# Performance work log

Measured on AMD Instinct MI355X. Metric: run time of the kernel, lower is better.

## Reference

```python
import jax, jax.numpy as jnp
import numpy as np

B, S, E, N = 2, 2048, 768, 12
H = E // N

def setup_inputs() -> dict:
    key = jax.random.key(0)
    k1, k2, k3, k4, k5 = jax.random.split(key, 5)
    x = jax.random.normal(k1, (B, S, E), dtype=jnp.float32)
    Wqkv = jax.random.normal(k2, (E, 3 * E), dtype=jnp.float32) * (1.0 / np.sqrt(E))
    bqkv = jax.random.normal(k3, (3 * E,), dtype=jnp.float32) * 0.02
    Wproj = jax.random.normal(k4, (E, E), dtype=jnp.float32) * (1.0 / np.sqrt(E))
    bproj = jax.random.normal(k5, (E,), dtype=jnp.float32) * 0.02
    mask = jnp.tril(jnp.ones((S, S), dtype=jnp.int32))[None, None]  # (1,1,S,S) causal
    return {"mask": mask, "x": x, "Wqkv": Wqkv, "bqkv": bqkv, "Wproj": Wproj, "bproj": bproj}

def reference(mask, x, Wqkv, bqkv, Wproj, bproj):
    Bx, Sx, Ex = x.shape
    Hd = Ex // N
    qkv = x @ Wqkv + bqkv                       # (B,S,3E)
    q, k, v = jnp.split(qkv, 3, axis=-1)
    q = q.reshape(Bx, Sx, N, Hd).transpose(0, 2, 1, 3)  # (B,N,S,H)
    k = k.reshape(Bx, Sx, N, Hd).transpose(0, 2, 1, 3)
    v = v.reshape(Bx, Sx, N, Hd).transpose(0, 2, 1, 3)
    att = jnp.einsum('bnsh,bnth->bnst', q, k) / jnp.sqrt(jnp.float32(Hd))
    att = jnp.where(mask == 0, -jnp.inf, att)   # causal masked_fill
    p = jax.nn.softmax(att, axis=-1)            # dropout p=0.0 -> identity
    y = jnp.einsum('bnst,bnth->bnsh', p, v)     # (B,N,S,H)
    y = y.transpose(0, 2, 1, 3).reshape(Bx, Sx, Ex)
    return y @ Wproj + bproj
```

## Files before the change

### kernel.cpp

```cpp
#include <hip/hip_runtime.h>
#include <math.h>

#define S_LEN 2048
#define E_DIM 768
#define NHEAD 12
#define HDIM 64
#define BATCH 2
#define MROWS (BATCH * S_LEN)
#define KDIM E_DIM
#define NBN (BATCH * NHEAD)
#define NTASKS 768

typedef __attribute__((ext_vector_type(8))) short bf16x8;
typedef __attribute__((ext_vector_type(4))) float f32x4;

__device__ inline unsigned short f2bf(float f) {
    union { float f; unsigned u; } v; v.f = f;
    unsigned r = (v.u + 0x7FFFu + ((v.u >> 16) & 1u)) >> 16;
    return (unsigned short)r;
}

__global__ __launch_bounds__(256) void prep(
    const float* __restrict__ x, unsigned short* __restrict__ Xb,
    const float* __restrict__ Wqkv, unsigned short* __restrict__ WqkvT,
    const float* __restrict__ Wproj, unsigned short* __restrict__ WprojT)
{
    __shared__ float t[32][33];
    const int blk = blockIdx.x, tid = threadIdx.x;
    if (blk < 3072) {
        const int i = blk * 256 + tid;
        const float4 a = ((const float4*)x)[i];
        ushort4 o;
        o.x = f2bf(a.x); o.y = f2bf(a.y); o.z = f2bf(a.z); o.w = f2bf(a.w);
        ((ushort4*)Xb)[i] = o;
        return;
    }
    const float* W; unsigned short* WT; int N, bt;
    if (blk < 3072 + 1728) { bt = blk - 3072; N = 3 * E_DIM; W = Wqkv; WT = WqkvT; }
    else                   { bt = blk - 4800; N = E_DIM;     W = Wproj; WT = WprojT; }
    const int bx = bt % (N / 32), by = bt / (N / 32);
    const int k0 = by * 32, n0 = bx * 32;
    const int r = tid >> 3, c4 = (tid & 7) * 4;
    const float4 v = *(const float4*)&W[(size_t)(k0 + r) * N + n0 + c4];
    t[r][c4 + 0] = v.x; t[r][c4 + 1] = v.y; t[r][c4 + 2] = v.z; t[r][c4 + 3] = v.w;
    __syncthreads();
    ushort4 o;
    o.x = f2bf(t[c4 + 0][r]); o.y = f2bf(t[c4 + 1][r]);
    o.z = f2bf(t[c4 + 2][r]); o.w = f2bf(t[c4 + 3][r]);
    *(ushort4*)&WT[(size_t)(n0 + r) * KDIM + k0 + c4] = o;
}

template <int EPI, int BM, int BN>
__global__ __launch_bounds__(256, 3) void gemm_t(
    const unsigned short* __restrict__ A, const unsigned short* __restrict__ BT,
    const float* __restrict__ bias, void* __restrict__ out0,
    void* __restrict__ out1, void* __restrict__ out2, int Nn)
{
    constexpr int MF = BM / 32;
    constexpr int NF = BN / 32;
    __shared__ unsigned short As[BM * 64];
    __shared__ unsigned short Bs[BN * 64];
    const int tid = threadIdx.x;
    const int lane = tid & 63;
    const int wid = tid >> 6;
    const int lr = lane & 15, lg = lane >> 4;
    const int wr = wid >> 1, wc = wid & 1;
    const int m0 = blockIdx.y * BM;
    const int n0 = blockIdx.x * BN;
    const int srow = lane >> 3, scol = (lane & 7) * 8;

    f32x4 acc[MF][NF];
    #pragma unroll
    for (int i = 0; i < MF; ++i)
        #pragma unroll
        for (int j = 0; j < NF; ++j) acc[i][j] = (f32x4){0.f, 0.f, 0.f, 0.f};

    for (int k0 = 0; k0 < KDIM; k0 += 64) {
        __syncthreads();
        #pragma unroll
        for (int c = 0; c < MF; ++c) {
            const int chunk = wid * MF + c;
            const int row = chunk * 8 + srow;
            const unsigned short* ga = A + (size_t)(m0 + row) * KDIM + k0 + scol;
            __builtin_amdgcn_global_load_lds(
                (const __attribute__((address_space(1))) void*)ga,
                (__attribute__((address_space(3))) void*)&As[chunk * 512], 16, 0, 0);
        }
        #pragma unroll
        for (int c = 0; c < NF; ++c) {
            const int chunk = wid * NF + c;
            const int row = chunk * 8 + srow;
            const unsigned short* gb = BT + (size_t)(n0 + row) * KDIM + k0 + scol;
            __builtin_amdgcn_global_load_lds(
                (const __attribute__((address_space(1))) void*)gb,
                (__attribute__((address_space(3))) void*)&Bs[chunk * 512], 16, 0, 0);
        }
        __syncthreads();

        #pragma unroll
        for (int kk = 0; kk < 2; ++kk) {
            bf16x8 af[MF], bf[NF];
            #pragma unroll
            for (int mt = 0; mt < MF; ++mt)
                af[mt] = *(const bf16x8*)&As[(wr * (BM / 2) + mt * 16 + lr) * 64 + kk * 32 + lg * 8];
            #pragma unroll
            for (int nt = 0; nt < NF; ++nt)
                bf[nt] = *(const bf16x8*)&Bs[(wc * (BN / 2) + nt * 16 + lr) * 64 + kk * 32 + lg * 8];
            #pragma unroll
            for (int mt = 0; mt < MF; ++mt)
                #pragma unroll
                for (int nt = 0; nt < NF; ++nt)
                    acc[mt][nt] = __builtin_amdgcn_mfma_f32_16x16x32_bf16(
                        af[mt], bf[nt], acc[mt][nt], 0, 0, 0);
        }
    }

    #pragma unroll
    for (int mt = 0; mt < MF; ++mt) {
        const int rowbase = m0 + wr * (BM / 2) + mt * 16 + lg * 4;
        #pragma unroll
        for (int nt = 0; nt < NF; ++nt) {
            const int col = n0 + wc * (BN / 2) + nt * 16 + lr;
            if (EPI == 0) {
                float* O = (float*)out0;
                const float bv = bias[col];
                #pragma unroll
                for (int r = 0; r < 4; ++r)
                    O[(size_t)(rowbase + r) * Nn + col] = acc[mt][nt][r] + bv;
            } else {
                const int which = col / E_DIM;
                const int rem = col % E_DIM;
                const int head = rem >> 6, h = rem & 63;
                const float bv = bias[col];
                if (which == 2) {
                    const int b = rowbase >> 11, s0 = rowbase & (S_LEN - 1);
                    const int scolv = (s0 & ~63) | ((s0 & 63) ^ ((h & 7) << 3));
                    unsigned short* VT = (unsigned short*)out2;
                    ushort4 pk;
                    pk.x = f2bf(acc[mt][nt][0] + bv);
                    pk.y = f2bf(acc[mt][nt][1] + bv);
                    pk.z = f2bf(acc[mt][nt][2] + bv);
                    pk.w = f2bf(acc[mt][nt][3] + bv);
                    *(ushort4*)&VT[((size_t)(b * NHEAD + head) * HDIM + h) * S_LEN + scolv] = pk;
                } else {
                    unsigned short* dst = (which == 0) ? (unsigned short*)out0
                                                       : (unsigned short*)out1;
                    const float sc = (which == 0) ? 0.125f : 1.0f;
                    #pragma unroll
                    for (int r = 0; r < 4; ++r) {
                        const int m = rowbase + r;
                        const int b = m >> 11, s = m & (S_LEN - 1);
                        const int hh = (which == 1) ? (h ^ ((s & 7) << 3)) : h;
                        dst[(((size_t)(b * NHEAD + head) * S_LEN) + s) * HDIM + hh] =
                            f2bf((acc[mt][nt][r] + bv) * sc);
                    }
                }
            }
        }
    }
}

__global__ __launch_bounds__(256) void attn_mfma(
    const unsigned short* __restrict__ Qb, const unsigned short* __restrict__ Kb,
    const unsigned short* __restrict__ VTb, unsigned short* __restrict__ Y,
    float* __restrict__ ws_o, float* __restrict__ ws_l)
{
    __shared__ unsigned short Ks[2][64 * 64];
    __shared__ unsigned short Vt[2][64 * 64];
    __shared__ unsigned short Ps[4 * 16 * 64];
    __shared__ float Ls[4][16];

    const int tid = threadIdx.x;
    const int lane = tid & 63;
    const int wid = tid >> 6;
    const int lr = lane & 15;
    const int lg = lane >> 4;

    const int task = blockIdx.x;
    const int bn = task % NBN;
    const int rest = task / NBN;
    const int jj = rest & 15, half = rest >> 4;
    const int b = bn / NHEAD, n = bn % NHEAD;

    const unsigned short* Kg = Kb + (size_t)bn * S_LEN * HDIM;
    const unsigned short* Vg = VTb + (size_t)bn * HDIM * S_LEN;

    auto run_pass = [&](int qb, int t0, int t1, int mode) {
        const size_t qoff = ((size_t)bn * S_LEN + (qb * 64 + wid * 16 + lr)) * HDIM;
        const bf16x8 qB0 = *(const bf16x8*)(Qb + qoff + lg * 8);
        const bf16x8 qB1 = *(const bf16x8*)(Qb + qoff + 32 + lg * 8);

        f32x4 o[4];
        #pragma unroll
        for (int ht = 0; ht < 4; ++ht) o[ht] = (f32x4){0.f, 0.f, 0.f, 0.f};
        float lacc = 0.f;

        __syncthreads();
        #pragma unroll
        for (int e = 0; e < 2; ++e) {
            const int chunk = wid * 2 + e;
            __builtin_amdgcn_global_load_lds(
                (const __attribute__((address_space(1))) void*)
                    (Kg + (size_t)t0 * 4096 + chunk * 512 + lane * 8),
                (__attribute__((address_space(3))) void*)&Ks[0][chunk * 512], 16, 0, 0);
            __builtin_amdgcn_global_load_lds(
                (const __attribute__((address_space(1))) void*)
                    (Vg + (size_t)(chunk * 8 + (lane >> 3)) * S_LEN + t0 * 64 + (lane & 7) * 8),
                (__attribute__((address_space(3))) void*)&Vt[0][chunk * 512], 16, 0, 0);
        }

        int cur = 0;
        for (int t = t0; t < t1; ++t) {
            __syncthreads();
            if (t + 1 < t1) {
                #pragma unroll
                for (int e = 0; e < 2; ++e) {
                    const int chunk = wid * 2 + e;
                    __builtin_amdgcn_global_load_lds(
                        (const __attribute__((address_space(1))) void*)
                            (Kg + (size_t)(t + 1) * 4096 + chunk * 512 + lane * 8),
                        (__attribute__((address_space(3))) void*)&Ks[cur ^ 1][chunk * 512],
                        16, 0, 0);
                    __builtin_amdgcn_global_load_lds(
                        (const __attribute__((address_space(1))) void*)
                            (Vg + (size_t)(chunk * 8 + (lane >> 3)) * S_LEN + (t + 1) * 64
                                + (lane & 7) * 8),
                        (__attribute__((address_space(3))) void*)&Vt[cur ^ 1][chunk * 512],
                        16, 0, 0);
                }
            }

            const unsigned short* Kc = Ks[cur];
            f32x4 s[4];
            __builtin_amdgcn_s_setprio(1);
            #pragma unroll
            for (int ct = 0; ct < 4; ++ct) {
                const int kr = ct * 16 + lr;
                const int xo = (kr & 7) << 3;
                const bf16x8 kb0 = *(const bf16x8*)&Kc[kr * 64 + ((lg * 8) ^ xo)];
                const bf16x8 kb1 = *(const bf16x8*)&Kc[kr * 64 + ((32 + lg * 8) ^ xo)];
                f32x4 a = (f32x4){0.f, 0.f, 0.f, 0.f};
                a = __builtin_amdgcn_mfma_f32_16x16x32_bf16(kb0, qB0, a, 0, 0, 0);
                a = __builtin_amdgcn_mfma_f32_16x16x32_bf16(kb1, qB1, a, 0, 0, 0);
                s[ct] = a;
            }
            __builtin_amdgcn_s_setprio(0);

            if (t == qb) {
                const int q = qb * 64 + wid * 16 + lr;
                #pragma unroll
                for (int ct = 0; ct < 4; ++ct) {
                    #pragma unroll
                    for (int r = 0; r < 4; ++r) {
                        const int k = t * 64 + ct * 16 + lg * 4 + r;
                        if (k > q) s[ct][r] = -1e30f;
                    }
                }
            }

            unsigned short* Pw = Ps + wid * 1024;
            const int pxo = (lr & 7) << 3;
            #pragma unroll
            for (int ct = 0; ct < 4; ++ct) {
                const float p0 = __expf(s[ct][0] - 8.f);
                const float p1 = __expf(s[ct][1] - 8.f);
                const float p2 = __expf(s[ct][2] - 8.f);
                const float p3 = __expf(s[ct][3] - 8.f);
                lacc += (p0 + p1) + (p2 + p3);
                ushort4 pk;
                pk.x = f2bf(p0); pk.y = f2bf(p1); pk.z = f2bf(p2); pk.w = f2bf(p3);
                *(ushort4*)&Pw[lr * 64 + ((ct * 16 + lg * 4) ^ pxo)] = pk;
            }

            const unsigned short* Vc = Vt[cur];
            const bf16x8 pa0 = *(const bf16x8*)&Pw[lr * 64 + ((lg * 8) ^ pxo)];
            const bf16x8 pa1 = *(const bf16x8*)&Pw[lr * 64 + ((32 + lg * 8) ^ pxo)];
            __builtin_amdgcn_s_setprio(1);
            #pragma unroll
            for (int ht = 0; ht < 4; ++ht) {
                const int h = ht * 16 + lr;
                const int xo = (h & 7) << 3;
                const bf16x8 vb0 = *(const bf16x8*)&Vc[h * 64 + ((lg * 8) ^ xo)];
                const bf16x8 vb1 = *(const bf16x8*)&Vc[h * 64 + ((32 + lg * 8) ^ xo)];
                o[ht] = __builtin_amdgcn_mfma_f32_16x16x32_bf16(pa0, vb0, o[ht], 0, 0, 0);
                o[ht] = __builtin_amdgcn_mfma_f32_16x16x32_bf16(pa1, vb1, o[ht], 0, 0, 0);
            }
            __builtin_amdgcn_s_setprio(0);
            cur ^= 1;
        }

        lacc += __shfl_xor(lacc, 16, 64);
        lacc += __shfl_xor(lacc, 32, 64);

        if (mode == 2) {
            if (lg == 0) Ls[wid][lr] = lacc;
            const float4 lv = *(const float4*)&Ls[wid][lg * 4];
            const float invl[4] = {1.f / lv.x, 1.f / lv.y, 1.f / lv.z, 1.f / lv.w};
            #pragma unroll
            for (int r = 0; r < 4; ++r) {
                const int qrow = qb * 64 + wid * 16 + lg * 4 + r;
                unsigned short* yrow =
                    Y + ((size_t)(b * S_LEN + qrow)) * E_DIM + n * HDIM;
                #pragma unroll
                for (int ht = 0; ht < 4; ++ht)
                    yrow[ht * 16 + lr] = f2bf(o[ht][r] * invl[r]);
            }
        } else {
            const size_t m = (size_t)(bn * 16 + (qb - 16)) * 2 + mode;
            float* wo = ws_o + m * 4096;
            const int rowl = wid * 16 + lg * 4;
            #pragma unroll
            for (int ht = 0; ht < 4; ++ht)
                #pragma unroll
                for (int r = 0; r < 4; ++r)
                    wo[(rowl + r) * 64 + ht * 16 + lr] = o[ht][r];
            if (lg == 0) ws_l[m * 64 + wid * 16 + lr] = lacc;
        }
    };

    if (half == 0) {
        run_pass(31 - jj, 0, 16, 0);
    } else {
        run_pass(31 - jj, 16, 32 - jj, 1);
        run_pass(jj, 0, jj + 1, 2);
    }
}

__global__ __launch_bounds__(256) void attn_merge(
    const float* __restrict__ ws_o, const float* __restrict__ ws_l,
    unsigned short* __restrict__ Y)
{
    const int m = blockIdx.x;
    const int bn = m / 16, qb = 16 + (m % 16);
    const int b = bn / NHEAD, n = bn % NHEAD;
    const int tid = threadIdx.x;
    const int r = tid >> 2, h0 = (tid & 3) * 16;

    const float* o0 = ws_o + ((size_t)m * 2 + 0) * 4096 + r * 64 + h0;
    const float* o1 = ws_o + ((size_t)m * 2 + 1) * 4096 + r * 64 + h0;
    const float l = ws_l[((size_t)m * 2 + 0) * 64 + r] +
                    ws_l[((size_t)m * 2 + 1) * 64 + r];
    const float inv = 1.f / l;
    unsigned short* yrow =
        Y + ((size_t)(b * S_LEN + qb * 64 + r)) * E_DIM + n * HDIM + h0;
    #pragma unroll
    for (int q = 0; q < 16; q += 4) {
        const float4 a = *(const float4*)(o0 + q);
        const float4 c = *(const float4*)(o1 + q);
        ushort4 pk;
        pk.x = f2bf((a.x + c.x) * inv); pk.y = f2bf((a.y + c.y) * inv);
        pk.z = f2bf((a.z + c.z) * inv); pk.w = f2bf((a.w + c.w) * inv);
        *(ushort4*)&yrow[q] = pk;
    }
}

extern "C" void kernel_launch(void* const* d_in, const int* in_sizes, int n_in,
                              void* d_out, int out_size, void* d_ws, size_t ws_size,
                              hipStream_t stream) {
    const float* x     = (const float*)d_in[1];
    const float* Wqkv  = (const float*)d_in[2];
    const float* bqkv  = (const float*)d_in[3];
    const float* Wproj = (const float*)d_in[4];
    const float* bproj = (const float*)d_in[5];
    float* out = (float*)d_out;

    const size_t per = (size_t)BATCH * NHEAD * S_LEN * HDIM;
    unsigned short* Xb     = (unsigned short*)d_ws;
    unsigned short* WqkvT  = Xb + (size_t)MROWS * E_DIM;
    unsigned short* WprojT = WqkvT + (size_t)3 * E_DIM * E_DIM;
    unsigned short* Qb     = WprojT + (size_t)E_DIM * E_DIM;
    unsigned short* Kb     = Qb + per;
    unsigned short* VTb    = Kb + per;
    unsigned short* Yb     = VTb + per;
    float*          ws_o   = (float*)(Yb + (size_t)MROWS * E_DIM);
    float*          ws_l   = ws_o + (size_t)384 * 2 * 4096;

    prep<<<5376, 256, 0, stream>>>(x, Xb, Wqkv, WqkvT, Wproj, WprojT);
    gemm_t<1, 128, 96><<<dim3(3 * E_DIM / 96, MROWS / 128), 256, 0, stream>>>(
        Xb, WqkvT, bqkv, Qb, Kb, VTb, 3 * E_DIM);
    attn_mfma<<<NTASKS, 256, 0, stream>>>(Qb, Kb, VTb, Yb, ws_o, ws_l);
    attn_merge<<<384, 256, 0, stream>>>(ws_o, ws_l, Yb);
    gemm_t<0, 64, 64><<<dim3(E_DIM / 64, MROWS / 64), 256, 0, stream>>>(
        Yb, WprojT, bproj, out, nullptr, nullptr, E_DIM);
}
```

Measured before the change: 84.20 us.

## Split attention warps 2x2 over query and key halves with shared P tile

Reorganizes the attention block's four waves from one 16-row query strip each into a 2x2 grid: each wave handles 32 query rows against 32 of the 64 keys per tile. K and V fragments read from LDS are reused across two query groups, which cuts LDS read traffic per MFMA. Partial outputs from the two key-half waves are reduced through shared memory at the end, and row sums go through a small LDS buffer. This adds extra barriers and an LDS reduction per pass, plus a shared P tile written and read across waves.

```diff
diff --git a/kernel.cpp b/kernel.cpp
--- a/kernel.cpp
+++ b/kernel.cpp
@@ -165,16 +165,18 @@
     const unsigned short* __restrict__ VTb, unsigned short* __restrict__ Y,
     float* __restrict__ ws_o, float* __restrict__ ws_l)
 {
-    __shared__ unsigned short Ks[2][64 * 64];
-    __shared__ unsigned short Vt[2][64 * 64];
-    __shared__ unsigned short Ps[4 * 16 * 64];
-    __shared__ float Ls[4][16];
+    __shared__ unsigned short smem[5 * 4096];
+    __shared__ float Lbuf[2][2][32];
 
     const int tid = threadIdx.x;
     const int lane = tid & 63;
     const int wid = tid >> 6;
     const int lr = lane & 15;
     const int lg = lane >> 4;
+    const int wq = wid >> 1;
+    const int wk = wid & 1;
+
+    unsigned short* const Ps = smem + 16384;
 
     const int task = blockIdx.x;
     const int bn = task % NBN;
@@ -186,14 +188,21 @@
     const unsigned short* Vg = VTb + (size_t)bn * HDIM * S_LEN;
 
     auto run_pass = [&](int qb, int t0, int t1, int mode) {
-        const size_t qoff = ((size_t)bn * S_LEN + (qb * 64 + wid * 16 + lr)) * HDIM;
-        const bf16x8 qB0 = *(const bf16x8*)(Qb + qoff + lg * 8);
-        const bf16x8 qB1 = *(const bf16x8*)(Qb + qoff + 32 + lg * 8);
-
-        f32x4 o[4];
-        #pragma unroll
-        for (int ht = 0; ht < 4; ++ht) o[ht] = (f32x4){0.f, 0.f, 0.f, 0.f};
-        float lacc = 0.f;
+        bf16x8 qB[2][2];
+        #pragma unroll
+        for (int qg = 0; qg < 2; ++qg) {
+            const size_t qoff =
+                ((size_t)bn * S_LEN + (qb * 64 + wq * 32 + qg * 16 + lr)) * HDIM;
+            qB[qg][0] = *(const bf16x8*)(Qb + qoff + lg * 8);
+            qB[qg][1] = *(const bf16x8*)(Qb + qoff + 32 + lg * 8);
+        }
+
+        f32x4 o[4][2];
+        #pragma unroll
+        for (int ht = 0; ht < 4; ++ht)
+            #pragma unroll
+            for (int qg = 0; qg < 2; ++qg) o[ht][qg] = (f32x4){0.f, 0.f, 0.f, 0.f};
+        float lacc[2] = {0.f, 0.f};
 
         __syncthreads();
         #pragma unroll
@@ -202,11 +211,11 @@
             __builtin_amdgcn_global_load_lds(
                 (const __attribute__((address_space(1))) void*)
                     (Kg + (size_t)t0 * 4096 + chunk * 512 + lane * 8),
-                (__attribute__((address_space(3))) void*)&Ks[0][chunk * 512], 16, 0, 0);
+                (__attribute__((address_space(3))) void*)&smem[chunk * 512], 16, 0, 0);
             __builtin_amdgcn_global_load_lds(
                 (const __attribute__((address_space(1))) void*)
                     (Vg + (size_t)(chunk * 8 + (lane >> 3)) * S_LEN + t0 * 64 + (lane & 7) * 8),
-                (__attribute__((address_space(3))) void*)&Vt[0][chunk * 512], 16, 0, 0);
+                (__attribute__((address_space(3))) void*)&smem[8192 + chunk * 512], 16, 0, 0);
         }
 
         int cur = 0;
@@ -219,102 +228,156 @@
                     __builtin_amdgcn_global_load_lds(
                         (const __attribute__((address_space(1))) void*)
                             (Kg + (size_t)(t + 1) * 4096 + chunk * 512 + lane * 8),
-                        (__attribute__((address_space(3))) void*)&Ks[cur ^ 1][chunk * 512],
-                        16, 0, 0);
+                        (__attribute__((address_space(3))) void*)
+                            &smem[(cur ^ 1) * 4096 + chunk * 512], 16, 0, 0);
                     __builtin_amdgcn_global_load_lds(
                         (const __attribute__((address_space(1))) void*)
                             (Vg + (size_t)(chunk * 8 + (lane >> 3)) * S_LEN + (t + 1) * 64
                                 + (lane & 7) * 8),
-                        (__attribute__((address_space(3))) void*)&Vt[cur ^ 1][chunk * 512],
-                        16, 0, 0);
+                        (__attribute__((address_space(3))) void*)
+                            &smem[8192 + (cur ^ 1) * 4096 + chunk * 512], 16, 0, 0);
                 }
             }
 
-            const unsigned short* Kc = Ks[cur];
-            f32x4 s[4];
+            const unsigned short* Kc = smem + cur * 4096;
+            const unsigned short* Vc = smem + 8192 + cur * 4096;
+
+            f32x4 s[2][2];
             __builtin_amdgcn_s_setprio(1);
             #pragma unroll
-            for (int ct = 0; ct < 4; ++ct) {
-                const int kr = ct * 16 + lr;
+            for (int kt = 0; kt < 2; ++kt) {
+                const int kr = wk * 32 + kt * 16 + lr;
                 const int xo = (kr & 7) << 3;
                 const bf16x8 kb0 = *(const bf16x8*)&Kc[kr * 64 + ((lg * 8) ^ xo)];
                 const bf16x8 kb1 = *(const bf16x8*)&Kc[kr * 64 + ((32 + lg * 8) ^ xo)];
-                f32x4 a = (f32x4){0.f, 0.f, 0.f, 0.f};
-                a = __builtin_amdgcn_mfma_f32_16x16x32_bf16(kb0, qB0, a, 0, 0, 0);
-                a = __builtin_amdgcn_mfma_f32_16x16x32_bf16(kb1, qB1, a, 0, 0, 0);
-                s[ct] = a;
+                #pragma unroll
+                for (int qg = 0; qg < 2; ++qg) {
+                    f32x4 a = (f32x4){0.f, 0.f, 0.f, 0.f};
+                    a = __builtin_amdgcn_mfma_f32_16x16x32_bf16(kb0, qB[qg][0], a, 0, 0, 0);
+                    a = __builtin_amdgcn_mfma_f32_16x16x32_bf16(kb1, qB[qg][1], a, 0, 0, 0);
+                    s[kt][qg] = a;
+                }
             }
             __builtin_amdgcn_s_setprio(0);
 
             if (t == qb) {
-                const int q = qb * 64 + wid * 16 + lr;
-                #pragma unroll
-                for (int ct = 0; ct < 4; ++ct) {
-                    #pragma unroll
-                    for (int r = 0; r < 4; ++r) {
-                        const int k = t * 64 + ct * 16 + lg * 4 + r;
-                        if (k > q) s[ct][r] = -1e30f;
+                #pragma unroll
+                for (int kt = 0; kt < 2; ++kt)
+                    #pragma unroll
+                    for (int qg = 0; qg < 2; ++qg) {
+                        const int q = qb * 64 + wq * 32 + qg * 16 + lr;
+                        #pragma unroll
+                        for (int r = 0; r < 4; ++r) {
+                            const int k = t * 64 + wk * 32 + kt * 16 + lg * 4 + r;
+                            if (k > q) s[kt][qg][r] = -1e30f;
+                        }
                     }
+            }
+
+            #pragma unroll
+            for (int kt = 0; kt < 2; ++kt)
+                #pragma unroll
+                for (int qg = 0; qg < 2; ++qg) {
+                    const float p0 = __expf(s[kt][qg][0] - 8.f);
+                    const float p1 = __expf(s[kt][qg][1] - 8.f);
+                    const float p2 = __expf(s[kt][qg][2] - 8.f);
+                    const float p3 = __expf(s[kt][qg][3] - 8.f);
+                    lacc[qg] += (p0 + p1) + (p2 + p3);
+                    ushort4 pk;
+                    pk.x = f2bf(p0); pk.y = f2bf(p1); pk.z = f2bf(p2); pk.w = f2bf(p3);
+                    const int prow = wq * 32 + qg * 16 + lr;
+                    const int pcol = wk * 32 + kt * 16 + lg * 4;
+                    *(ushort4*)&Ps[prow * 64 + (pcol ^ ((prow & 7) << 3))] = pk;
                 }
-            }
-
-            unsigned short* Pw = Ps + wid * 1024;
-            const int pxo = (lr & 7) << 3;
-            #pragma unroll
-            for (int ct = 0; ct < 4; ++ct) {
-                const float p0 = __expf(s[ct][0] - 8.f);
-                const float p1 = __expf(s[ct][1] - 8.f);
-                const float p2 = __expf(s[ct][2] - 8.f);
-                const float p3 = __expf(s[ct][3] - 8.f);
-                lacc += (p0 + p1) + (p2 + p3);
-                ushort4 pk;
-                pk.x = f2bf(p0); pk.y = f2bf(p1); pk.z = f2bf(p2); pk.w = f2bf(p3);
-                *(ushort4*)&Pw[lr * 64 + ((ct * 16 + lg * 4) ^ pxo)] = pk;
-            }
-
-            const unsigned short* Vc = Vt[cur];
-            const bf16x8 pa0 = *(const bf16x8*)&Pw[lr * 64 + ((lg * 8) ^ pxo)];
-            const bf16x8 pa1 = *(const bf16x8*)&Pw[lr * 64 + ((32 + lg * 8) ^ pxo)];
+
+            bf16x8 pa[2];
+            #pragma unroll
+            for (int qg = 0; qg < 2; ++qg) {
+                const int prow = wq * 32 + qg * 16 + lr;
+                pa[qg] = *(const bf16x8*)
+                    &Ps[prow * 64 + ((wk * 32 + lg * 8) ^ ((prow & 7) << 3))];
+            }
             __builtin_amdgcn_s_setprio(1);
             #pragma unroll
             for (int ht = 0; ht < 4; ++ht) {
                 const int h = ht * 16 + lr;
                 const int xo = (h & 7) << 3;
-                const bf16x8 vb0 = *(const bf16x8*)&Vc[h * 64 + ((lg * 8) ^ xo)];
-                const bf16x8 vb1 = *(const bf16x8*)&Vc[h * 64 + ((32 + lg * 8) ^ xo)];
-                o[ht] = __builtin_amdgcn_mfma_f32_16x16x32_bf16(pa0, vb0, o[ht], 0, 0, 0);
-                o[ht] = __builtin_amdgcn_mfma_f32_16x16x32_bf16(pa1, vb1, o[ht], 0, 0, 0);
+                const bf16x8 vb = *(const bf16x8*)
+                    &Vc[h * 64 + ((wk * 32 + lg * 8) ^ xo)];
+                #pragma unroll
+                for (int qg = 0; qg < 2; ++qg)
+                    o[ht][qg] = __builtin_amdgcn_mfma_f32_16x16x32_bf16(
+                        pa[qg], vb, o[ht][qg], 0, 0, 0);
             }
             __builtin_amdgcn_s_setprio(0);
             cur ^= 1;
         }
 
-        lacc += __shfl_xor(lacc, 16, 64);
-        lacc += __shfl_xor(lacc, 32, 64);
-
-        if (mode == 2) {
-            if (lg == 0) Ls[wid][lr] = lacc;
-            const float4 lv = *(const float4*)&Ls[wid][lg * 4];
-            const float invl[4] = {1.f / lv.x, 1.f / lv.y, 1.f / lv.z, 1.f / lv.w};
-            #pragma unroll
-            for (int r = 0; r < 4; ++r) {
-                const int qrow = qb * 64 + wid * 16 + lg * 4 + r;
-                unsigned short* yrow =
-                    Y + ((size_t)(b * S_LEN + qrow)) * E_DIM + n * HDIM;
-                #pragma unroll
-                for (int ht = 0; ht < 4; ++ht)
-                    yrow[ht * 16 + lr] = f2bf(o[ht][r] * invl[r]);
-            }
-        } else {
-            const size_t m = (size_t)(bn * 16 + (qb - 16)) * 2 + mode;
-            float* wo = ws_o + m * 4096;
-            const int rowl = wid * 16 + lg * 4;
+        #pragma unroll
+        for (int qg = 0; qg < 2; ++qg) {
+            lacc[qg] += __shfl_xor(lacc[qg], 16, 64);
+            lacc[qg] += __shfl_xor(lacc[qg], 32, 64);
+        }
+        if (lg == 0) {
+            Lbuf[wq][wk][lr] = lacc[0];
+            Lbuf[wq][wk][16 + lr] = lacc[1];
+        }
+
+        __syncthreads();
+        float* const Ox = (float*)smem;
+        if (wk == 1) {
             #pragma unroll
             for (int ht = 0; ht < 4; ++ht)
                 #pragma unroll
-                for (int r = 0; r < 4; ++r)
-                    wo[(rowl + r) * 64 + ht * 16 + lr] = o[ht][r];
-            if (lg == 0) ws_l[m * 64 + wid * 16 + lr] = lacc;
+                for (int qg = 0; qg < 2; ++qg)
+                    #pragma unroll
+                    for (int r = 0; r < 4; ++r)
+                        Ox[(wq * 32 + qg * 16 + lg * 4 + r) * 68 + ht * 16 + lr] =
+                            o[ht][qg][r];
+        }
+        __syncthreads();
+        if (wk == 0) {
+            #pragma unroll
+            for (int ht = 0; ht < 4; ++ht)
+                #pragma unroll
+                for (int qg = 0; qg < 2; ++qg)
+                    #pragma unroll
+                    for (int r = 0; r < 4; ++r)
+                        o[ht][qg][r] +=
+                            Ox[(wq * 32 + qg * 16 + lg * 4 + r) * 68 + ht * 16 + lr];
+
+            if (mode == 2) {
+                #pragma unroll
+                for (int qg = 0; qg < 2; ++qg)
+                    #pragma unroll
+                    for (int r = 0; r < 4; ++r) {
+                        const int ql = qg * 16 + lg * 4 + r;
+                        const float inv =
+                            1.f / (Lbuf[wq][0][ql] + Lbuf[wq][1][ql]);
+                        const int qrow = qb * 64 + wq * 32 + ql;
+                        unsigned short* yrow =
+                            Y + ((size_t)(b * S_LEN + qrow)) * E_DIM + n * HDIM;
+                        #pragma unroll
+                        for (int ht = 0; ht < 4; ++ht)
+                            yrow[ht * 16 + lr] = f2bf(o[ht][qg][r] * inv);
+                    }
+            } else {
+                const size_t m = (size_t)(bn * 16 + (qb - 16)) * 2 + mode;
+                float* wo = ws_o + m * 4096;
+                #pragma unroll
+                for (int qg = 0; qg < 2; ++qg)
+                    #pragma unroll
+                    for (int r = 0; r < 4; ++r) {
+                        const int ql = qg * 16 + lg * 4 + r;
+                        const int rowl = wq * 32 + ql;
+                        #pragma unroll
+                        for (int ht = 0; ht < 4; ++ht)
+                            wo[rowl * 64 + ht * 16 + lr] = o[ht][qg][r];
+                        if (lr == 0)
+                            ws_l[m * 64 + rowl] =
+                                Lbuf[wq][0][ql] + Lbuf[wq][1][ql];
+                    }
+            }
         }
     };
 
```

After: 85.24 us. Within noise of the previous version (+1.2%).
